# Kernel tuning notes

Measured on AMD Instinct MI355X. Metric: run time of the kernel, lower is better.

## Reference

```python
import jax, jax.numpy as jnp
import numpy as np

N_NODES = 100000
N_EDGES = 1200000
N_GRAPHS = 256
IN_CH = 7
HID = 64
OUT_CH = 10


def setup_inputs() -> dict:
    key = jax.random.key(0)
    ks = jax.random.split(key, 12)
    x = jax.random.normal(ks[0], (N_NODES, IN_CH), dtype=jnp.float32)
    edge_index = jax.random.randint(ks[1], (2, N_EDGES), 0, N_NODES, dtype=jnp.int64)
    batch = jnp.sort(jax.random.randint(ks[2], (N_NODES,), 0, N_GRAPHS, dtype=jnp.int64))
    def glorot(k, shape):
        lim = np.sqrt(6.0 / (shape[0] + shape[1]))
        return jax.random.uniform(k, shape, dtype=jnp.float32, minval=-lim, maxval=lim)
    return {
        "x": x,
        "edge_index": edge_index,
        "batch": batch,
        "W0": glorot(ks[3], (IN_CH, HID)),
        "b0": jnp.zeros((HID,), jnp.float32),
        "W1": glorot(ks[4], (HID, HID)),
        "b1": jnp.zeros((HID,), jnp.float32),
        "W2": glorot(ks[5], (HID, HID)),
        "b2": jnp.zeros((HID,), jnp.float32),
        "lin_W": glorot(ks[6], (HID, OUT_CH)),
        "lin_b": jnp.zeros((OUT_CH,), jnp.float32),
    }


def _gcn_conv(h, W, b, src, dst, dis):
    # GCNConv: D^{-1/2}(A+I)D^{-1/2} h W + b, with self-loops added implicitly.
    hw = h @ W  # [N, HID]
    norm = dis[src] * dis[dst]  # [E]
    agg = jax.ops.segment_sum(norm[:, None] * hw[src], dst, num_segments=h.shape[0])
    agg = agg + (dis * dis)[:, None] * hw  # self-loop term
    return agg + b


def reference(x, edge_index, batch, W0, b0, W1, b1, W2, b2, lin_W, lin_b):
    src, dst = edge_index[0], edge_index[1]
    n = x.shape[0]
    # symmetric normalization degrees (incl. self-loop), computed on targets
    deg = jax.ops.segment_sum(jnp.ones(src.shape[0], x.dtype), dst, num_segments=n) + 1.0
    dis = jax.lax.rsqrt(deg)
    h = jax.nn.relu(_gcn_conv(x, W0, b0, src, dst, dis))
    h = jax.nn.relu(_gcn_conv(h, W1, b1, src, dst, dis))
    h = _gcn_conv(h, W2, b2, src, dst, dis)
    # global_mean_pool over batch assignment
    sums = jax.ops.segment_sum(h, batch, num_segments=N_GRAPHS)
    cnt = jax.ops.segment_sum(jnp.ones(n, h.dtype), batch, num_segments=N_GRAPHS)
    pooled = sums / jnp.maximum(cnt, 1.0)[:, None]  # [N_GRAPHS, HID]
    return pooled @ lin_W + lin_b  # [N_GRAPHS, OUT_CH]
```

## Files before the change

kernel.cpp:

```cpp
#include <hip/hip_runtime.h>

#define NN 100000
#define NE 1200000
#define NG 256
#define INC 7
#define HID 64
#define OUTC 10

#define NBKT 196
#define BCAP 8192
#define BIN_CHUNK 4096
#define NBIN_BLK ((NE + BIN_CHUNK - 1) / BIN_CHUNK)
#define EPT (BIN_CHUNK / 256)
#define NBLK64 ((NN + 63) / 64)

typedef unsigned int uint;
typedef unsigned short ushort;

__device__ inline uint pk2bf(float a, float b) {
    uint ua = __float_as_uint(a);
    ua = (ua + 0x7fffu + ((ua >> 16) & 1u)) >> 16;
    uint ub = __float_as_uint(b);
    ub = (ub + 0x7fffu + ((ub >> 16) & 1u)) & 0xffff0000u;
    return ua | ub;
}
__device__ inline ushort f2bf(float f) {
    uint u = __float_as_uint(f);
    return (ushort)((u + 0x7fffu + ((u >> 16) & 1u)) >> 16);
}
__device__ inline void acc8(float* a, uint4 r) {
    a[0] += __uint_as_float(r.x << 16); a[1] += __uint_as_float(r.x & 0xffff0000u);
    a[2] += __uint_as_float(r.y << 16); a[3] += __uint_as_float(r.y & 0xffff0000u);
    a[4] += __uint_as_float(r.z << 16); a[5] += __uint_as_float(r.z & 0xffff0000u);
    a[6] += __uint_as_float(r.w << 16); a[7] += __uint_as_float(r.w & 0xffff0000u);
}
__device__ inline float4 cvt4(uint2 r) {
    float4 f;
    f.x = __uint_as_float(r.x << 16); f.y = __uint_as_float(r.x & 0xffff0000u);
    f.z = __uint_as_float(r.y << 16); f.w = __uint_as_float(r.y & 0xffff0000u);
    return f;
}


__global__ void k_zero(float* __restrict__ sums, float* __restrict__ cnt,
                       int* __restrict__ bktcur) {
    int i = blockIdx.x * blockDim.x + threadIdx.x;
    if (i < NG * 16) sums[i] = 0.0f;
    if (i < NG) cnt[i] = 0.0f;
    if (i < NBKT) bktcur[i] = 0;
}


__global__ __launch_bounds__(256) void k_bin(const int* __restrict__ src,
                                             const int* __restrict__ dst,
                                             int* __restrict__ bktcur,
                                             uint* __restrict__ binned) {
    __shared__ int hcnt[NBKT];
    __shared__ int hbase[NBKT];
    int tid = threadIdx.x;
    int e0 = blockIdx.x * BIN_CHUNK;
    int lim = NE - e0; if (lim > BIN_CHUNK) lim = BIN_CHUNK;

    int dr[EPT], sr[EPT];
    for (int b = tid; b < NBKT; b += 256) hcnt[b] = 0;
    __syncthreads();
#pragma unroll
    for (int u = 0; u < EPT; ++u) {
        int i = tid + u * 256;
        bool ok = i < lim;
        dr[u] = ok ? dst[e0 + i] : -1;
        sr[u] = ok ? src[e0 + i] : 0;
        if (ok) atomicAdd(&hcnt[dr[u] >> 9], 1);
    }
    __syncthreads();
    for (int b = tid; b < NBKT; b += 256) {
        int c = hcnt[b];
        hbase[b] = c ? atomicAdd(&bktcur[b], c) : 0;
        hcnt[b] = 0;
    }
    __syncthreads();
#pragma unroll
    for (int u = 0; u < EPT; ++u) {
        if (dr[u] >= 0) {
            int b = dr[u] >> 9;
            int r = atomicAdd(&hcnt[b], 1);
            binned[(size_t)b * BCAP + hbase[b] + r] = ((uint)sr[u] << 9) | (dr[u] & 511);
        }
    }
}


__global__ __launch_bounds__(256) void k_build(const uint* __restrict__ binned,
                                               const int* __restrict__ bktcur,
                                               int* __restrict__ csr,
                                               int* __restrict__ rowptr,
                                               int* __restrict__ cnts,
                                               float* __restrict__ dis,
                                               const float* __restrict__ x,
                                               float* __restrict__ xp) {
    __shared__ int lcnt[512];
    __shared__ int lcur[512];
    __shared__ int sa[512], sb[512];
    __shared__ int s_base, s_m;
    int b = blockIdx.x;
    int tid = threadIdx.x;
    int nbase = b << 9;
    int nnum = NN - nbase; if (nnum > 512) nnum = 512;

    {
        int v = (tid < NBKT) ? bktcur[tid] : 0;
        sa[tid] = v;
        __syncthreads();
        int* p = sa; int* q = sb;
        for (int off = 1; off < 256; off <<= 1) {
            q[tid] = p[tid] + ((tid >= off) ? p[tid - off] : 0);
            __syncthreads();
            int* t2 = p; p = q; q = t2;
        }
        if (tid == b) { s_base = p[tid] - v; s_m = v; }
        __syncthreads();
    }
    int m = s_m;
    int base = s_base;
    const uint* bp = binned + (size_t)b * BCAP;

    for (int n = tid; n < 512; n += 256) lcnt[n] = 0;
    __syncthreads();
    for (int i = tid; i < m; i += 256) atomicAdd(&lcnt[bp[i] & 511], 1);
    __syncthreads();
    for (int n = tid; n < 512; n += 256) sa[n] = lcnt[n];
    __syncthreads();
    int* p = sa; int* q = sb;
    for (int off = 1; off < 512; off <<= 1) {
        for (int n = tid; n < 512; n += 256)
            q[n] = p[n] + ((n >= off) ? p[n - off] : 0);
        __syncthreads();
        int* t2 = p; p = q; q = t2;
    }
    for (int n = tid; n < 512; n += 256) {
        int pre = p[n] - lcnt[n];
        lcur[n] = pre;
        if (n < nnum) {
            int c = lcnt[n];
            rowptr[nbase + n] = base + pre;
            cnts[nbase + n] = c;
            dis[nbase + n] = rsqrtf((float)c + 1.0f);
        }
    }
    __syncthreads();
    for (int i = tid; i < m; i += 256) {
        uint pk = bp[i];
        int ld = pk & 511;
        int s = (int)(pk >> 9);
        int r = atomicAdd(&lcur[ld], 1);
        csr[base + r] = s;
    }
    for (int i = tid; i < (nnum << 3); i += 256) {
        int n = i >> 3, c = i & 7;
        float dv = rsqrtf((float)lcnt[n] + 1.0f);
        xp[(((size_t)(nbase + n)) << 3) + c] =
            (c < INC) ? dv * x[(size_t)(nbase + n) * INC + c] : 0.0f;
    }
}


__global__ __launch_bounds__(256) void k_l01(const float* __restrict__ xp,
                                             const int* __restrict__ csr,
                                             const int* __restrict__ rowptr,
                                             const int* __restrict__ cnts,
                                             const float* __restrict__ dis,
                                             const float* __restrict__ W0,
                                             const float* __restrict__ b0,
                                             const float* __restrict__ W1,
                                             ushort* __restrict__ hwpb) {
    __shared__ float sW0[INC][HID];
    __shared__ float sW1[HID][HID];
    __shared__ float sx[64][8];
    __shared__ float h0T[HID][HID + 4];
    __shared__ float sdis[64];
    __shared__ float sb0[HID];
    int tid = threadIdx.x;
    int n0 = blockIdx.x * 64;

    for (int i = tid; i < INC * HID; i += 256) sW0[i >> 6][i & 63] = W0[i];
    for (int i = tid; i < HID * HID; i += 256) sW1[i >> 6][i & 63] = W1[i];
    if (tid < 64) {
        sb0[tid] = b0[tid];
        sdis[tid] = (n0 + tid < NN) ? dis[n0 + tid] : 0.0f;
    }
    {
        int dl = tid >> 2, l = tid & 3;
        int d = n0 + dl;
        float2 a0 = {0.f, 0.f}, a1 = {0.f, 0.f};
        if (d < NN) {
            int beg = rowptr[d], num = cnts[d];
            a0 = ((const float2*)&xp[(size_t)d * 8])[l];
            int j = 0;
            while (j < num) {
                int chunk = min(num - j, 4);
                int iv = (l < chunk) ? csr[beg + j + l] : 0;
                int k = 0;
                for (; k + 2 <= chunk; k += 2) {
                    int s0 = __shfl(iv, k, 4);
                    int s1 = __shfl(iv, k + 1, 4);
                    float2 r0 = ((const float2*)&xp[(size_t)s0 * 8])[l];
                    float2 r1 = ((const float2*)&xp[(size_t)s1 * 8])[l];
                    a0.x += r0.x; a0.y += r0.y;
                    a1.x += r1.x; a1.y += r1.y;
                }
                for (; k < chunk; ++k) {
                    int s = __shfl(iv, k, 4);
                    float2 r = ((const float2*)&xp[(size_t)s * 8])[l];
                    a0.x += r.x; a0.y += r.y;
                }
                j += chunk;
            }
        }
        float dd = (tid >> 2) < 64 ? 0.0f : 0.0f;
        (void)dd;
        float ds = ((n0 + (tid >> 2)) < NN) ? dis[n0 + (tid >> 2)] : 0.0f;
        sx[dl][l * 2]     = ds * (a0.x + a1.x);
        sx[dl][l * 2 + 1] = ds * (a0.y + a1.y);
    }
    __syncthreads();
    {
        int tn = tid >> 4, tc = tid & 15;
        float acc[4][4] = {};
#pragma unroll
        for (int k = 0; k < INC; ++k) {
            float hv[4];
#pragma unroll
            for (int i = 0; i < 4; ++i) hv[i] = sx[tn * 4 + i][k];
            float4 w4 = *(const float4*)&sW0[k][tc * 4];
            float wv[4] = {w4.x, w4.y, w4.z, w4.w};
#pragma unroll
            for (int i = 0; i < 4; ++i)
#pragma unroll
                for (int j = 0; j < 4; ++j)
                    acc[i][j] = fmaf(hv[i], wv[j], acc[i][j]);
        }
#pragma unroll
        for (int i = 0; i < 4; ++i)
#pragma unroll
            for (int j = 0; j < 4; ++j)
                h0T[tc * 4 + j][tn * 4 + i] = fmaxf(acc[i][j] + sb0[tc * 4 + j], 0.0f);
    }
    __syncthreads();
    {
        int tn = tid >> 4, tc = tid & 15;
        float acc[4][4] = {};
#pragma unroll 8
        for (int k = 0; k < HID; ++k) {
            float4 h4 = *(const float4*)&h0T[k][tn * 4];
            float4 w4 = *(const float4*)&sW1[k][tc * 4];
            float hv[4] = {h4.x, h4.y, h4.z, h4.w};
            float wv[4] = {w4.x, w4.y, w4.z, w4.w};
#pragma unroll
            for (int i = 0; i < 4; ++i)
#pragma unroll
                for (int j = 0; j < 4; ++j)
                    acc[i][j] = fmaf(hv[i], wv[j], acc[i][j]);
        }
#pragma unroll
        for (int i = 0; i < 4; ++i) {
            int gn = n0 + tn * 4 + i;
            if (gn < NN) {
                float dsc = sdis[tn * 4 + i];
                uint2 o;
                o.x = pk2bf(dsc * acc[i][0], dsc * acc[i][1]);
                o.y = pk2bf(dsc * acc[i][2], dsc * acc[i][3]);
                ((uint2*)(hwpb + (size_t)gn * 64))[tc] = o;
            }
        }
    }
}


__global__ __launch_bounds__(512) void k_l2(const ushort* __restrict__ hwpb,
                                            const int* __restrict__ csr,
                                            const int* __restrict__ rowptr,
                                            const int* __restrict__ cnts,
                                            const float* __restrict__ dis,
                                            const float* __restrict__ b1,
                                            const float* __restrict__ W2,
                                            const float* __restrict__ linW,
                                            ushort* __restrict__ zb) {
    __shared__ float sWc[HID][16];
    __shared__ float h1T[HID][HID + 4];
    __shared__ float sdis[64];
    __shared__ float sb1[HID];
    int tid = threadIdx.x;
    int n0 = blockIdx.x * 64;

    for (int i = tid; i < HID * 16; i += 512) {
        int k = i >> 4, o = i & 15;
        float acc = 0.0f;
        if (o < OUTC)
            for (int q = 0; q < HID; ++q) acc += W2[k * HID + q] * linW[q * OUTC + o];
        sWc[k][o] = acc;
    }
    if (tid < 64) {
        sb1[tid] = b1[tid];
        sdis[tid] = (n0 + tid < NN) ? dis[n0 + tid] : 0.0f;
    }
    {
        int dl = tid >> 3, l = tid & 7;
        int d = n0 + dl;
        float a0[8] = {}, a1[8] = {};
        if (d < NN) {
            int beg = rowptr[d], num = cnts[d];
            acc8(a0, ((const uint4*)(hwpb + (size_t)d * 64))[l]);
            int j = 0;
            while (j < num) {
                int chunk = min(num - j, 8);
                int iv = (l < chunk) ? csr[beg + j + l] : 0;
                int k = 0;
                for (; k + 2 <= chunk; k += 2) {
                    int s0 = __shfl(iv, k, 8);
                    int s1 = __shfl(iv, k + 1, 8);
                    uint4 r0 = ((const uint4*)(hwpb + (size_t)s0 * 64))[l];
                    uint4 r1 = ((const uint4*)(hwpb + (size_t)s1 * 64))[l];
                    acc8(a0, r0);
                    acc8(a1, r1);
                }
                if (k < chunk) {
                    int s = __shfl(iv, k, 8);
                    acc8(a0, ((const uint4*)(hwpb + (size_t)s * 64))[l]);
                }
                j += chunk;
            }
            float dd = sdis[dl];
#pragma unroll
            for (int i = 0; i < 8; ++i) {
                float v = fmaxf(dd * (a0[i] + a1[i]) + sb1[l * 8 + i], 0.0f);
                h1T[l * 8 + i][dl] = v;
            }
        } else {
#pragma unroll
            for (int i = 0; i < 8; ++i) h1T[l * 8 + i][dl] = 0.0f;
        }
    }
    __syncthreads();
    if (tid < 256) {
        int nq = tid >> 4, c = tid & 15;
        float acc[4] = {};
#pragma unroll 8
        for (int k = 0; k < HID; ++k) {
            float4 h4 = *(const float4*)&h1T[k][nq * 4];
            float w = sWc[k][c];
            acc[0] = fmaf(h4.x, w, acc[0]);
            acc[1] = fmaf(h4.y, w, acc[1]);
            acc[2] = fmaf(h4.z, w, acc[2]);
            acc[3] = fmaf(h4.w, w, acc[3]);
        }
#pragma unroll
        for (int i = 0; i < 4; ++i) {
            int gn = n0 + nq * 4 + i;
            if (gn < NN) zb[(size_t)gn * 16 + c] = f2bf(sdis[nq * 4 + i] * acc[i]);
        }
    }
}


__global__ __launch_bounds__(256) void k_l3pool(const ushort* __restrict__ zb,
                                                const int* __restrict__ csr,
                                                const int* __restrict__ rowptr,
                                                const int* __restrict__ cnts,
                                                const float* __restrict__ dis,
                                                const int* __restrict__ batch,
                                                float* __restrict__ sums,
                                                float* __restrict__ cnt) {
    __shared__ float lsum[16][16];
    __shared__ int lcnt_[16];
    __shared__ int s_gmin;
    int tid = threadIdx.x;
    int n0 = blockIdx.x * 64;
    if (tid < 256) lsum[tid >> 4][tid & 15] = 0.0f;
    if (tid < 16) lcnt_[tid] = 0;
    if (tid == 0) s_gmin = batch[n0];
    __syncthreads();

    int dl = tid >> 2, l = tid & 3;
    int d = n0 + dl;
    if (d < NN) {
        int beg = rowptr[d], num = cnts[d];
        float4 a0 = cvt4(((const uint2*)(zb + (size_t)d * 16))[l]);
        float4 a1 = {0.f, 0.f, 0.f, 0.f};
        int j = 0;
        while (j < num) {
            int chunk = min(num - j, 4);
            int iv = (l < chunk) ? csr[beg + j + l] : 0;
            int k = 0;
            for (; k + 2 <= chunk; k += 2) {
                int s0 = __shfl(iv, k, 4);
                int s1 = __shfl(iv, k + 1, 4);
                float4 r0 = cvt4(((const uint2*)(zb + (size_t)s0 * 16))[l]);
                float4 r1 = cvt4(((const uint2*)(zb + (size_t)s1 * 16))[l]);
                a0.x += r0.x; a0.y += r0.y; a0.z += r0.z; a0.w += r0.w;
                a1.x += r1.x; a1.y += r1.y; a1.z += r1.z; a1.w += r1.w;
            }
            for (; k < chunk; ++k) {
                int s = __shfl(iv, k, 4);
                float4 r = cvt4(((const uint2*)(zb + (size_t)s * 16))[l]);
                a0.x += r.x; a0.y += r.y; a0.z += r.z; a0.w += r.w;
            }
            j += chunk;
        }
        float dd = dis[d];
        float4 v = {dd * (a0.x + a1.x), dd * (a0.y + a1.y),
                    dd * (a0.z + a1.z), dd * (a0.w + a1.w)};
        int g = batch[d];
        int slot = g - s_gmin;
        if (slot >= 0 && slot < 16) {
            atomicAdd(&lsum[slot][l * 4 + 0], v.x);
            atomicAdd(&lsum[slot][l * 4 + 1], v.y);
            atomicAdd(&lsum[slot][l * 4 + 2], v.z);
            atomicAdd(&lsum[slot][l * 4 + 3], v.w);
            if (l == 0) atomicAdd(&lcnt_[slot], 1);
        } else {
            atomicAdd(&sums[g * 16 + l * 4 + 0], v.x);
            atomicAdd(&sums[g * 16 + l * 4 + 1], v.y);
            atomicAdd(&sums[g * 16 + l * 4 + 2], v.z);
            atomicAdd(&sums[g * 16 + l * 4 + 3], v.w);
            if (l == 0) atomicAdd(&cnt[g], 1.0f);
        }
    }
    __syncthreads();
    {
        int slot = tid >> 4, c = tid & 15;
        if (lcnt_[slot] > 0) {
            atomicAdd(&sums[(s_gmin + slot) * 16 + c], lsum[slot][c]);
            if (c == 0) atomicAdd(&cnt[s_gmin + slot], (float)lcnt_[slot]);
        }
    }
}


__global__ void k_final2(const float* __restrict__ sums, const float* __restrict__ cnt,
                         const float* __restrict__ b2, const float* __restrict__ linW,
                         const float* __restrict__ linb, float* __restrict__ out) {
    int t = blockIdx.x * blockDim.x + threadIdx.x;
    if (t < NG * OUTC) {
        int g = t / OUTC, o = t % OUTC;
        float bc = linb[o];
        for (int q = 0; q < HID; ++q) bc += b2[q] * linW[q * OUTC + o];
        out[t] = sums[g * 16 + o] / fmaxf(cnt[g], 1.0f) + bc;
    }
}


extern "C" void kernel_launch(void* const* d_in, const int* in_sizes, int n_in,
                              void* d_out, int out_size, void* d_ws, size_t ws_size,
                              hipStream_t stream) {
    const float* x     = (const float*)d_in[0];
    const int*   ei    = (const int*)d_in[1];
    const int*   src   = ei;
    const int*   dst   = ei + NE;
    const int*   batch = (const int*)d_in[2];
    const float* W0 = (const float*)d_in[3];
    const float* b0 = (const float*)d_in[4];
    const float* W1 = (const float*)d_in[5];
    const float* b1 = (const float*)d_in[6];
    const float* W2 = (const float*)d_in[7];
    const float* b2 = (const float*)d_in[8];
    const float* linW = (const float*)d_in[9];
    const float* linb = (const float*)d_in[10];
    float* out = (float*)d_out;

    char* ws = (char*)d_ws;
    float*  xp     = (float*)ws;    ws += sizeof(float) * NN * 8;
    ushort* hwpb   = (ushort*)ws;   ws += sizeof(ushort) * NN * HID;
    ushort* zb     = (ushort*)ws;   ws += sizeof(ushort) * NN * 16;
    float*  dis    = (float*)ws;    ws += sizeof(float) * NN;
    float*  sums   = (float*)ws;    ws += sizeof(float) * NG * 16;
    float*  cnt    = (float*)ws;    ws += sizeof(float) * NG;
    int*    cnts   = (int*)ws;      ws += sizeof(int) * NN;
    int*    rowptr = (int*)ws;      ws += sizeof(int) * NN;
    int*    bktcur = (int*)ws;      ws += sizeof(int) * NBKT;
    uint*   binned = (uint*)ws;     ws += sizeof(uint) * NBKT * BCAP;
    int*    csr    = (int*)ws;      ws += sizeof(int) * NE;

    const int TB = 256;

    k_zero<<<16, TB, 0, stream>>>(sums, cnt, bktcur);
    k_bin<<<NBIN_BLK, TB, 0, stream>>>(src, dst, bktcur, binned);
    k_build<<<NBKT, TB, 0, stream>>>(binned, bktcur, csr, rowptr, cnts, dis, x, xp);

    k_l01<<<NBLK64, TB, 0, stream>>>(xp, csr, rowptr, cnts, dis, W0, b0, W1, hwpb);

    k_l2<<<NBLK64, 512, 0, stream>>>(hwpb, csr, rowptr, cnts, dis, b1, W2, linW, zb);

    k_l3pool<<<NBLK64, TB, 0, stream>>>(zb, csr, rowptr, cnts, dis, batch, sums, cnt);

    k_final2<<<(NG * OUTC + TB - 1) / TB, TB, 0, stream>>>(sums, cnt, b2, linW, linb, out);
}
```

Baseline: 224.4 us.

## Pad CSR rows to multiples of eight with dummy zero node, unroll gathers

Rebuilds the CSR so each row is padded to a multiple of eight entries using a sentinel node index NN, whose feature rows are zeroed in the extended buffers. This lets the three gather kernels use fixed 8-wide unrolled loops with no tail handling and more loads in flight. It also gives each bucket a fixed CSR region, which removes the per-block prefix scan in k_build, and moves the W2·linW precompute into k_zero so each k_l2 block no longer redoes it. In exchange, the padding adds extra gather traffic (about 3.5 wasted entries per row on average at about 12 edges per node) and needs a larger CSR buffer.

```diff
diff --git a/kernel.cpp b/kernel.cpp
--- a/kernel.cpp
+++ b/kernel.cpp
@@ -9,6 +9,7 @@
 
 #define NBKT 196
 #define BCAP 8192
+#define CSRCAP 10240
 #define BIN_CHUNK 4096
 #define NBIN_BLK ((NE + BIN_CHUNK - 1) / BIN_CHUNK)
 #define EPT (BIN_CHUNK / 256)
@@ -34,20 +35,31 @@
     a[4] += __uint_as_float(r.z << 16); a[5] += __uint_as_float(r.z & 0xffff0000u);
     a[6] += __uint_as_float(r.w << 16); a[7] += __uint_as_float(r.w & 0xffff0000u);
 }
-__device__ inline float4 cvt4(uint2 r) {
-    float4 f;
-    f.x = __uint_as_float(r.x << 16); f.y = __uint_as_float(r.x & 0xffff0000u);
-    f.z = __uint_as_float(r.y << 16); f.w = __uint_as_float(r.y & 0xffff0000u);
-    return f;
+__device__ inline void acc4(float4& a, uint2 r) {
+    a.x += __uint_as_float(r.x << 16); a.y += __uint_as_float(r.x & 0xffff0000u);
+    a.z += __uint_as_float(r.y << 16); a.w += __uint_as_float(r.y & 0xffff0000u);
 }
 
 
 __global__ void k_zero(float* __restrict__ sums, float* __restrict__ cnt,
-                       int* __restrict__ bktcur) {
+                       int* __restrict__ bktcur, float* __restrict__ xp,
+                       ushort* __restrict__ hwpb, ushort* __restrict__ zb,
+                       const float* __restrict__ W2, const float* __restrict__ linW,
+                       float* __restrict__ wsWc) {
     int i = blockIdx.x * blockDim.x + threadIdx.x;
     if (i < NG * 16) sums[i] = 0.0f;
     if (i < NG) cnt[i] = 0.0f;
     if (i < NBKT) bktcur[i] = 0;
+    if (i < 8) xp[(size_t)NN * 8 + i] = 0.0f;
+    if (i < 64) hwpb[(size_t)NN * 64 + i] = 0;
+    if (i < 16) zb[(size_t)NN * 16 + i] = 0;
+    if (i < HID * 16) {
+        int k = i >> 4, o = i & 15;
+        float acc = 0.0f;
+        if (o < OUTC)
+            for (int q = 0; q < HID; ++q) acc += W2[k * HID + q] * linW[q * OUTC + o];
+        wsWc[i] = acc;
+    }
 }
 
 
@@ -101,34 +113,19 @@
     __shared__ int lcnt[512];
     __shared__ int lcur[512];
     __shared__ int sa[512], sb[512];
-    __shared__ int s_base, s_m;
     int b = blockIdx.x;
     int tid = threadIdx.x;
     int nbase = b << 9;
     int nnum = NN - nbase; if (nnum > 512) nnum = 512;
-
-    {
-        int v = (tid < NBKT) ? bktcur[tid] : 0;
-        sa[tid] = v;
-        __syncthreads();
-        int* p = sa; int* q = sb;
-        for (int off = 1; off < 256; off <<= 1) {
-            q[tid] = p[tid] + ((tid >= off) ? p[tid - off] : 0);
-            __syncthreads();
-            int* t2 = p; p = q; q = t2;
-        }
-        if (tid == b) { s_base = p[tid] - v; s_m = v; }
-        __syncthreads();
-    }
-    int m = s_m;
-    int base = s_base;
+    int m = bktcur[b];
     const uint* bp = binned + (size_t)b * BCAP;
+    int csrbase = b * CSRCAP;
 
     for (int n = tid; n < 512; n += 256) lcnt[n] = 0;
     __syncthreads();
     for (int i = tid; i < m; i += 256) atomicAdd(&lcnt[bp[i] & 511], 1);
     __syncthreads();
-    for (int n = tid; n < 512; n += 256) sa[n] = lcnt[n];
+    for (int n = tid; n < 512; n += 256) sa[n] = (lcnt[n] + 7) & ~7;
     __syncthreads();
     int* p = sa; int* q = sb;
     for (int off = 1; off < 512; off <<= 1) {
@@ -138,11 +135,12 @@
         int* t2 = p; p = q; q = t2;
     }
     for (int n = tid; n < 512; n += 256) {
-        int pre = p[n] - lcnt[n];
+        int c = lcnt[n];
+        int pad = (c + 7) & ~7;
+        int pre = p[n] - pad;
         lcur[n] = pre;
         if (n < nnum) {
-            int c = lcnt[n];
-            rowptr[nbase + n] = base + pre;
+            rowptr[nbase + n] = csrbase + pre;
             cnts[nbase + n] = c;
             dis[nbase + n] = rsqrtf((float)c + 1.0f);
         }
@@ -153,7 +151,13 @@
         int ld = pk & 511;
         int s = (int)(pk >> 9);
         int r = atomicAdd(&lcur[ld], 1);
-        csr[base + r] = s;
+        csr[csrbase + r] = s;
+    }
+    __syncthreads();
+    for (int n = tid; n < 512; n += 256) {
+        int c = lcnt[n];
+        int endp = (lcur[n] - c) + ((c + 7) & ~7);
+        for (int k = lcur[n]; k < endp; ++k) csr[csrbase + k] = NN;
     }
     for (int i = tid; i < (nnum << 3); i += 256) {
         int n = i >> 3, c = i & 7;
@@ -191,36 +195,36 @@
     {
         int dl = tid >> 2, l = tid & 3;
         int d = n0 + dl;
-        float2 a0 = {0.f, 0.f}, a1 = {0.f, 0.f};
+        float2 a0 = {0.f, 0.f}, a1 = {0.f, 0.f}, a2 = {0.f, 0.f}, a3 = {0.f, 0.f};
+        float ds = 0.0f;
         if (d < NN) {
-            int beg = rowptr[d], num = cnts[d];
+            int beg = rowptr[d];
+            int npad = (cnts[d] + 7) & ~7;
             a0 = ((const float2*)&xp[(size_t)d * 8])[l];
-            int j = 0;
-            while (j < num) {
-                int chunk = min(num - j, 4);
-                int iv = (l < chunk) ? csr[beg + j + l] : 0;
-                int k = 0;
-                for (; k + 2 <= chunk; k += 2) {
-                    int s0 = __shfl(iv, k, 4);
-                    int s1 = __shfl(iv, k + 1, 4);
-                    float2 r0 = ((const float2*)&xp[(size_t)s0 * 8])[l];
-                    float2 r1 = ((const float2*)&xp[(size_t)s1 * 8])[l];
-                    a0.x += r0.x; a0.y += r0.y;
-                    a1.x += r1.x; a1.y += r1.y;
-                }
-                for (; k < chunk; ++k) {
-                    int s = __shfl(iv, k, 4);
-                    float2 r = ((const float2*)&xp[(size_t)s * 8])[l];
-                    a0.x += r.x; a0.y += r.y;
-                }
-                j += chunk;
+            for (int j = 0; j < npad; j += 8) {
+                int iv0 = csr[beg + j + l];
+                int iv1 = csr[beg + j + 4 + l];
+                int s0 = __shfl(iv0, 0, 4), s1 = __shfl(iv0, 1, 4);
+                int s2 = __shfl(iv0, 2, 4), s3 = __shfl(iv0, 3, 4);
+                int s4 = __shfl(iv1, 0, 4), s5 = __shfl(iv1, 1, 4);
+                int s6 = __shfl(iv1, 2, 4), s7 = __shfl(iv1, 3, 4);
+                float2 r0 = ((const float2*)&xp[(size_t)s0 * 8])[l];
+                float2 r1 = ((const float2*)&xp[(size_t)s1 * 8])[l];
+                float2 r2 = ((const float2*)&xp[(size_t)s2 * 8])[l];
+                float2 r3 = ((const float2*)&xp[(size_t)s3 * 8])[l];
+                float2 r4 = ((const float2*)&xp[(size_t)s4 * 8])[l];
+                float2 r5 = ((const float2*)&xp[(size_t)s5 * 8])[l];
+                float2 r6 = ((const float2*)&xp[(size_t)s6 * 8])[l];
+                float2 r7 = ((const float2*)&xp[(size_t)s7 * 8])[l];
+                a0.x += r0.x; a0.y += r0.y;  a1.x += r1.x; a1.y += r1.y;
+                a2.x += r2.x; a2.y += r2.y;  a3.x += r3.x; a3.y += r3.y;
+                a0.x += r4.x; a0.y += r4.y;  a1.x += r5.x; a1.y += r5.y;
+                a2.x += r6.x; a2.y += r6.y;  a3.x += r7.x; a3.y += r7.y;
             }
-        }
-        float dd = (tid >> 2) < 64 ? 0.0f : 0.0f;
-        (void)dd;
-        float ds = ((n0 + (tid >> 2)) < NN) ? dis[n0 + (tid >> 2)] : 0.0f;
-        sx[dl][l * 2]     = ds * (a0.x + a1.x);
-        sx[dl][l * 2 + 1] = ds * (a0.y + a1.y);
+            ds = dis[d];
+        }
+        sx[dl][l * 2]     = ds * ((a0.x + a1.x) + (a2.x + a3.x));
+        sx[dl][l * 2 + 1] = ds * ((a0.y + a1.y) + (a2.y + a3.y));
     }
     __syncthreads();
     {
@@ -282,8 +286,7 @@
                                             const int* __restrict__ cnts,
                                             const float* __restrict__ dis,
                                             const float* __restrict__ b1,
-                                            const float* __restrict__ W2,
-                                            const float* __restrict__ linW,
+                                            const float* __restrict__ wsWc,
                                             ushort* __restrict__ zb) {
     __shared__ float sWc[HID][16];
     __shared__ float h1T[HID][HID + 4];
@@ -292,48 +295,41 @@
     int tid = threadIdx.x;
     int n0 = blockIdx.x * 64;
 
-    for (int i = tid; i < HID * 16; i += 512) {
-        int k = i >> 4, o = i & 15;
-        float acc = 0.0f;
-        if (o < OUTC)
-            for (int q = 0; q < HID; ++q) acc += W2[k * HID + q] * linW[q * OUTC + o];
-        sWc[k][o] = acc;
-    }
+    for (int i = tid; i < HID * 16; i += 512) sWc[i >> 4][i & 15] = wsWc[i];
     if (tid < 64) {
         sb1[tid] = b1[tid];
         sdis[tid] = (n0 + tid < NN) ? dis[n0 + tid] : 0.0f;
     }
+    __syncthreads();
     {
         int dl = tid >> 3, l = tid & 7;
         int d = n0 + dl;
-        float a0[8] = {}, a1[8] = {};
         if (d < NN) {
-            int beg = rowptr[d], num = cnts[d];
+            float a0[8] = {}, a1[8] = {};
+            int beg = rowptr[d];
+            int npad = (cnts[d] + 7) & ~7;
             acc8(a0, ((const uint4*)(hwpb + (size_t)d * 64))[l]);
-            int j = 0;
-            while (j < num) {
-                int chunk = min(num - j, 8);
-                int iv = (l < chunk) ? csr[beg + j + l] : 0;
-                int k = 0;
-                for (; k + 2 <= chunk; k += 2) {
-                    int s0 = __shfl(iv, k, 8);
-                    int s1 = __shfl(iv, k + 1, 8);
-                    uint4 r0 = ((const uint4*)(hwpb + (size_t)s0 * 64))[l];
-                    uint4 r1 = ((const uint4*)(hwpb + (size_t)s1 * 64))[l];
-                    acc8(a0, r0);
-                    acc8(a1, r1);
-                }
-                if (k < chunk) {
-                    int s = __shfl(iv, k, 8);
-                    acc8(a0, ((const uint4*)(hwpb + (size_t)s * 64))[l]);
-                }
-                j += chunk;
+            for (int j = 0; j < npad; j += 8) {
+                int iv = csr[beg + j + l];
+                int s0 = __shfl(iv, 0, 8), s1 = __shfl(iv, 1, 8);
+                int s2 = __shfl(iv, 2, 8), s3 = __shfl(iv, 3, 8);
+                int s4 = __shfl(iv, 4, 8), s5 = __shfl(iv, 5, 8);
+                int s6 = __shfl(iv, 6, 8), s7 = __shfl(iv, 7, 8);
+                uint4 r0 = ((const uint4*)(hwpb + (size_t)s0 * 64))[l];
+                uint4 r1 = ((const uint4*)(hwpb + (size_t)s1 * 64))[l];
+                uint4 r2 = ((const uint4*)(hwpb + (size_t)s2 * 64))[l];
+                uint4 r3 = ((const uint4*)(hwpb + (size_t)s3 * 64))[l];
+                uint4 r4 = ((const uint4*)(hwpb + (size_t)s4 * 64))[l];
+                uint4 r5 = ((const uint4*)(hwpb + (size_t)s5 * 64))[l];
+                uint4 r6 = ((const uint4*)(hwpb + (size_t)s6 * 64))[l];
+                uint4 r7 = ((const uint4*)(hwpb + (size_t)s7 * 64))[l];
+                acc8(a0, r0); acc8(a1, r1); acc8(a0, r2); acc8(a1, r3);
+                acc8(a0, r4); acc8(a1, r5); acc8(a0, r6); acc8(a1, r7);
             }
             float dd = sdis[dl];
 #pragma unroll
             for (int i = 0; i < 8; ++i) {
-                float v = fmaxf(dd * (a0[i] + a1[i]) + sb1[l * 8 + i], 0.0f);
-                h1T[l * 8 + i][dl] = v;
+                h1T[l * 8 + i][dl] = fmaxf(dd * (a0[i] + a1[i]) + sb1[l * 8 + i], 0.0f);
             }
         } else {
 #pragma unroll
@@ -383,32 +379,34 @@
     int dl = tid >> 2, l = tid & 3;
     int d = n0 + dl;
     if (d < NN) {
-        int beg = rowptr[d], num = cnts[d];
-        float4 a0 = cvt4(((const uint2*)(zb + (size_t)d * 16))[l]);
-        float4 a1 = {0.f, 0.f, 0.f, 0.f};
-        int j = 0;
-        while (j < num) {
-            int chunk = min(num - j, 4);
-            int iv = (l < chunk) ? csr[beg + j + l] : 0;
-            int k = 0;
-            for (; k + 2 <= chunk; k += 2) {
-                int s0 = __shfl(iv, k, 4);
-                int s1 = __shfl(iv, k + 1, 4);
-                float4 r0 = cvt4(((const uint2*)(zb + (size_t)s0 * 16))[l]);
-                float4 r1 = cvt4(((const uint2*)(zb + (size_t)s1 * 16))[l]);
-                a0.x += r0.x; a0.y += r0.y; a0.z += r0.z; a0.w += r0.w;
-                a1.x += r1.x; a1.y += r1.y; a1.z += r1.z; a1.w += r1.w;
-            }
-            for (; k < chunk; ++k) {
-                int s = __shfl(iv, k, 4);
-                float4 r = cvt4(((const uint2*)(zb + (size_t)s * 16))[l]);
-                a0.x += r.x; a0.y += r.y; a0.z += r.z; a0.w += r.w;
-            }
-            j += chunk;
+        int beg = rowptr[d];
+        int npad = (cnts[d] + 7) & ~7;
+        float4 a0 = {0.f, 0.f, 0.f, 0.f}, a1 = {0.f, 0.f, 0.f, 0.f};
+        float4 a2 = {0.f, 0.f, 0.f, 0.f}, a3 = {0.f, 0.f, 0.f, 0.f};
+        acc4(a0, ((const uint2*)(zb + (size_t)d * 16))[l]);
+        for (int j = 0; j < npad; j += 8) {
+            int iv0 = csr[beg + j + l];
+            int iv1 = csr[beg + j + 4 + l];
+            int s0 = __shfl(iv0, 0, 4), s1 = __shfl(iv0, 1, 4);
+            int s2 = __shfl(iv0, 2, 4), s3 = __shfl(iv0, 3, 4);
+            int s4 = __shfl(iv1, 0, 4), s5 = __shfl(iv1, 1, 4);
+            int s6 = __shfl(iv1, 2, 4), s7 = __shfl(iv1, 3, 4);
+            uint2 r0 = ((const uint2*)(zb + (size_t)s0 * 16))[l];
+            uint2 r1 = ((const uint2*)(zb + (size_t)s1 * 16))[l];
+            uint2 r2 = ((const uint2*)(zb + (size_t)s2 * 16))[l];
+            uint2 r3 = ((const uint2*)(zb + (size_t)s3 * 16))[l];
+            uint2 r4 = ((const uint2*)(zb + (size_t)s4 * 16))[l];
+            uint2 r5 = ((const uint2*)(zb + (size_t)s5 * 16))[l];
+            uint2 r6 = ((const uint2*)(zb + (size_t)s6 * 16))[l];
+            uint2 r7 = ((const uint2*)(zb + (size_t)s7 * 16))[l];
+            acc4(a0, r0); acc4(a1, r1); acc4(a2, r2); acc4(a3, r3);
+            acc4(a0, r4); acc4(a1, r5); acc4(a2, r6); acc4(a3, r7);
         }
         float dd = dis[d];
-        float4 v = {dd * (a0.x + a1.x), dd * (a0.y + a1.y),
-                    dd * (a0.z + a1.z), dd * (a0.w + a1.w)};
+        float4 v = {dd * ((a0.x + a1.x) + (a2.x + a3.x)),
+                    dd * ((a0.y + a1.y) + (a2.y + a3.y)),
+                    dd * ((a0.z + a1.z) + (a2.z + a3.z)),
+                    dd * ((a0.w + a1.w) + (a2.w + a3.w))};
         int g = batch[d];
         int slot = g - s_gmin;
         if (slot >= 0 && slot < 16) {
@@ -468,27 +466,28 @@
     float* out = (float*)d_out;
 
     char* ws = (char*)d_ws;
-    float*  xp     = (float*)ws;    ws += sizeof(float) * NN * 8;
-    ushort* hwpb   = (ushort*)ws;   ws += sizeof(ushort) * NN * HID;
-    ushort* zb     = (ushort*)ws;   ws += sizeof(ushort) * NN * 16;
+    float*  xp     = (float*)ws;    ws += sizeof(float) * (NN + 1) * 8;
+    ushort* hwpb   = (ushort*)ws;   ws += sizeof(ushort) * (NN + 1) * HID;
+    ushort* zb     = (ushort*)ws;   ws += sizeof(ushort) * (NN + 1) * 16;
     float*  dis    = (float*)ws;    ws += sizeof(float) * NN;
     float*  sums   = (float*)ws;    ws += sizeof(float) * NG * 16;
     float*  cnt    = (float*)ws;    ws += sizeof(float) * NG;
+    float*  wsWc   = (float*)ws;    ws += sizeof(float) * HID * 16;
     int*    cnts   = (int*)ws;      ws += sizeof(int) * NN;
     int*    rowptr = (int*)ws;      ws += sizeof(int) * NN;
     int*    bktcur = (int*)ws;      ws += sizeof(int) * NBKT;
     uint*   binned = (uint*)ws;     ws += sizeof(uint) * NBKT * BCAP;
-    int*    csr    = (int*)ws;      ws += sizeof(int) * NE;
+    int*    csr    = (int*)ws;      ws += sizeof(int) * NBKT * CSRCAP;
 
     const int TB = 256;
 
-    k_zero<<<16, TB, 0, stream>>>(sums, cnt, bktcur);
+    k_zero<<<16, TB, 0, stream>>>(sums, cnt, bktcur, xp, hwpb, zb, W2, linW, wsWc);
     k_bin<<<NBIN_BLK, TB, 0, stream>>>(src, dst, bktcur, binned);
     k_build<<<NBKT, TB, 0, stream>>>(binned, bktcur, csr, rowptr, cnts, dis, x, xp);
 
     k_l01<<<NBLK64, TB, 0, stream>>>(xp, csr, rowptr, cnts, dis, W0, b0, W1, hwpb);
 
-    k_l2<<<NBLK64, 512, 0, stream>>>(hwpb, csr, rowptr, cnts, dis, b1, W2, linW, zb);
+    k_l2<<<NBLK64, 512, 0, stream>>>(hwpb, csr, rowptr, cnts, dis, b1, wsWc, zb);
 
     k_l3pool<<<NBLK64, TB, 0, stream>>>(zb, csr, rowptr, cnts, dis, batch, sums, cnt);
 
```

New measurement: 220.7 us. About the same (-1.7%).
